# Kernel tuning notes

Measured on AMD Instinct MI355X. Metric: run time of the kernel, lower is better.

The kernel has to match this reference:

```python
import jax, jax.numpy as jnp
import numpy as np

N_NODES = 20000
SEQ_T = 24
EMB = 64
H_LSTM = 128
H_GCN = 128
OUT = 16
N_CAT = 20000
N_EDGE = 640000


def setup_inputs() -> dict:
    key = jax.random.key(0)
    ks = jax.random.split(key, 16)
    s = 0.05
    emb = jax.random.normal(ks[4], (N_CAT + 1, EMB), jnp.float32) * s
    emb = emb.at[0].set(0.0)  # padding_idx=0
    inp = {
        "x_tokens": jax.random.randint(ks[0], (N_NODES, SEQ_T), 0, N_CAT + 1, dtype=jnp.int32),
        "lengths": jax.random.randint(ks[1], (N_NODES,), 1, SEQ_T + 1, dtype=jnp.int32),
        "edge_index": jax.random.randint(ks[2], (2, N_EDGE), 0, N_NODES, dtype=jnp.int32),
        "edge_weight": jax.random.uniform(ks[3], (N_EDGE,), jnp.float32, 0.1, 1.0),
        "emb": emb,
        "W_ih": jax.random.normal(ks[5], (4 * H_LSTM, EMB), jnp.float32) * s,
        "W_hh": jax.random.normal(ks[6], (4 * H_LSTM, H_LSTM), jnp.float32) * s,
        "b_ih": jax.random.normal(ks[7], (4 * H_LSTM,), jnp.float32) * s,
        "b_hh": jax.random.normal(ks[8], (4 * H_LSTM,), jnp.float32) * s,
        "conv1_W": jax.random.normal(ks[9], (H_LSTM, H_GCN), jnp.float32) * s,
        "conv1_b": jax.random.normal(ks[10], (H_GCN,), jnp.float32) * s,
        "conv2_W": jax.random.normal(ks[11], (H_GCN, H_GCN), jnp.float32) * s,
        "conv2_b": jax.random.normal(ks[12], (H_GCN,), jnp.float32) * s,
        "fc_W": jax.random.normal(ks[13], (H_GCN, OUT), jnp.float32) * s,
        "fc_b": jax.random.normal(ks[14], (OUT,), jnp.float32) * s,
    }
    return inp


def _lstm_last(xseq, lengths, W_ih, W_hh, b):
    # xseq: [N, T, E]; unidirectional LSTM -> output at t=len-1 equals
    # pack_padded_sequence result (causality). PyTorch gate order: i, f, g, o.
    n = xseq.shape[0]
    h0 = jnp.zeros((n, H_LSTM), xseq.dtype)

    def step(carry, xt):
        h, c = carry
        z = xt @ W_ih.T + h @ W_hh.T + b  # [N, 4H]
        i, f, g, o = jnp.split(z, 4, axis=-1)
        c = jax.nn.sigmoid(f) * c + jax.nn.sigmoid(i) * jnp.tanh(g)
        h = jax.nn.sigmoid(o) * jnp.tanh(c)
        return (h, c), h

    _, hs = jax.lax.scan(step, (h0, h0), jnp.swapaxes(xseq, 0, 1))  # hs: [T, N, H]
    return hs[lengths - 1, jnp.arange(n)]  # [N, H]


def _gcn_conv(x, W, b, src, dst, w, n):
    # PyG GCNConv: self loops (weight 1) + symmetric normalization.
    h = x @ W  # [N, G]
    deg = jax.ops.segment_sum(w, dst, num_segments=n) + 1.0
    dinv = jax.lax.rsqrt(deg)
    norm = dinv[src] * w * dinv[dst]  # [E]
    agg = jax.ops.segment_sum(h[src] * norm[:, None], dst, num_segments=n)
    agg = agg + h * (dinv * dinv)[:, None]  # self-loop term
    return agg + b


def reference(x_tokens, lengths, edge_index, edge_weight, emb, W_ih, W_hh,
              b_ih, b_hh, conv1_W, conv1_b, conv2_W, conv2_b, fc_W, fc_b):
    n = x_tokens.shape[0]
    src, dst = edge_index[0], edge_index[1]
    xe = emb[x_tokens]  # [N, T, E]
    x = _lstm_last(xe, lengths, W_ih, W_hh, b_ih + b_hh)  # [N, H_LSTM]
    x = jax.nn.relu(_gcn_conv(x, conv1_W, conv1_b, src, dst, edge_weight, n))
    # dropout: identity (eval mode)
    x = jax.nn.relu(_gcn_conv(x, conv2_W, conv2_b, src, dst, edge_weight, n))
    return x @ fc_W + fc_b  # [N, OUT]
```

## Files before the change

### kernel.cpp

```cpp
#include <hip/hip_runtime.h>
#include <math.h>

#define N_NODES 20000
#define SEQ_T   24
#define EMBD    64
#define HL      128
#define OUTF    16
#define NEDGE   640000
#define G4      512
#define KTOT    192
#define ROWS    80
#define RF      5
#define NBLSTM  250
#define LDA     232
#define WSTRIDE 12288

#define NBCSR   250
#define EPB     (NEDGE/NBCSR)
#define NPB     (N_NODES/NBCSR)
#define CSRT    1024

#define CROWS   64
#define CRF     4
#define NCBLK   313
#define CPAD    136

typedef __bf16 bf16x8 __attribute__((ext_vector_type(8)));
typedef __bf16 bf16x2 __attribute__((ext_vector_type(2)));
typedef float  f32x4  __attribute__((ext_vector_type(4)));
typedef unsigned short u16;

__device__ __forceinline__ float4 ld4(const float* p){ return *reinterpret_cast<const float4*>(p); }
__device__ __forceinline__ void st4(float* p, float4 v){ *reinterpret_cast<float4*>(p) = v; }

#define LOG2E 1.44269504f

#define S_EMB   320016
#define S_WTP   (S_EMB + KTOT*G4)
#define S_C1    (S_WTP + 16384)
#define S_C2    (S_C1 + 16384)
#define S_BIAS  (S_C2 + G4)
#define PREPBLK ((S_BIAS + 255)/256)

__global__ __launch_bounds__(256) void prep_all(
    const float* __restrict__ emb,  __bf16* __restrict__ embb,
    const float* __restrict__ Wih,  const float* __restrict__ Whh,
    __bf16* __restrict__ WTp,
    const float* __restrict__ c1W,  __bf16* __restrict__ wc1b,
    const float* __restrict__ c2W,  __bf16* __restrict__ wc2b,
    const float* __restrict__ bi,   const float* __restrict__ bh,
    float* __restrict__ bs)
{
    int gid = blockIdx.x*256 + threadIdx.x;
    if (gid < S_EMB) {
        int i4 = gid*4;
        float4 v = ld4(emb + i4);
        embb[i4+0] = (__bf16)v.x;
        embb[i4+1] = (__bf16)v.y;
        embb[i4+2] = (__bf16)v.z;
        embb[i4+3] = (__bf16)v.w;
    } else if (gid < S_WTP) {
        int idx = gid - S_EMB;
        int ko = idx & 31;
        int c  = (idx >> 5) & 15;
        int gt = (idx >> 9) & 3;
        int kc = (idx >> 11) % 6;
        int w  = idx / WSTRIDE;
        int g  = gt*HL + w*16 + c;
        int kk = kc*32 + ko;
        float v = (kk < EMBD) ? Wih[g*EMBD + kk] : Whh[g*HL + (kk - EMBD)];
        WTp[idx] = (__bf16)v;
    } else if (gid < S_C2) {
        bool c2 = (gid >= S_C1);
        int idx = gid - (c2 ? S_C1 : S_WTP);
        const float* W = c2 ? c2W : c1W;
        __bf16* dst = c2 ? wc2b : wc1b;
        int ko = idx & 31;
        int c  = (idx >> 5) & 15;
        int kc = (idx >> 9) & 3;
        int w  = idx >> 11;
        int g  = w*16 + c;
        int k  = kc*32 + ko;
        dst[idx] = (__bf16)W[k*HL + g];
    } else if (gid < S_BIAS) {
        int i = gid - S_C2;
        bs[i] = bi[i] + bh[i];
    }
}

__global__ __launch_bounds__(CSRT) void csr_count(
    const int* __restrict__ esrc, const int* __restrict__ edst,
    const float* __restrict__ ew,
    int* __restrict__ rank, u16* __restrict__ gcnt, float* __restrict__ gdeg)
{
    __shared__ int   hist[N_NODES];
    __shared__ float fdeg[N_NODES];
    const int tid = threadIdx.x, bid = blockIdx.x;
    const int e0 = bid * EPB;

    uint4* h4 = reinterpret_cast<uint4*>(hist);
    uint4* f4 = reinterpret_cast<uint4*>(fdeg);
    for (int i = tid; i < N_NODES/4; i += CSRT) {
        h4[i] = make_uint4(0,0,0,0);
        f4[i] = make_uint4(0,0,0,0);
    }
    __syncthreads();

    #pragma unroll
    for (int k = 0; k < 3; ++k) {
        int i = tid + CSRT*k;
        if (k < 2 || i < EPB) {
            int e = e0 + i;
            int d = edst[e];
            rank[e] = atomicAdd(&hist[d], 1);
            atomicAdd(&fdeg[d], ew[e]);
        }
    }
    __syncthreads();

    for (int i = tid; i < N_NODES; i += CSRT) {
        gcnt[(size_t)bid*N_NODES + i] = (u16)hist[i];
        gdeg[(size_t)bid*N_NODES + i] = fdeg[i];
    }
}

__global__ __launch_bounds__(CSRT) void csr_scan(
    u16* __restrict__ gcnt, const float* __restrict__ gdeg,
    float* __restrict__ dinv, int* __restrict__ tot)
{
    __shared__ u16   ctile[NBCSR*NPB];
    __shared__ float dtile[NBCSR*NPB];
    const int tid = threadIdx.x, bid = blockIdx.x;
    const int nodes0 = bid * NPB;

    for (int idx = tid; idx < NBCSR*NPB; idx += CSRT) {
        int b = idx / NPB, i = idx - b*NPB;
        ctile[idx] = gcnt[(size_t)b*N_NODES + nodes0 + i];
        dtile[idx] = gdeg[(size_t)b*N_NODES + nodes0 + i];
    }
    __syncthreads();
    if (tid < NPB) {
        int run = 0; float dsum = 0.f;
        for (int b = 0; b < NBCSR; ++b) {
            int v = ctile[b*NPB + tid];
            ctile[b*NPB + tid] = (u16)run;
            run += v;
            dsum += dtile[b*NPB + tid];
        }
        tot[nodes0 + tid]  = run;
        dinv[nodes0 + tid] = rsqrtf(dsum + 1.0f);
    }
    __syncthreads();
    for (int idx = tid; idx < NBCSR*NPB; idx += CSRT) {
        int b = idx / NPB, i = idx - b*NPB;
        gcnt[(size_t)b*N_NODES + nodes0 + i] = ctile[idx];
    }
}

__global__ __launch_bounds__(256) void csr_rowstart(const int* __restrict__ tot,
                                                    int* __restrict__ row_start)
{
    __shared__ int part[NBCSR];
    const int t = threadIdx.x;
    if (t < NBCSR) {
        int s = 0;
        for (int i = 0; i < NPB; ++i) s += tot[t*NPB + i];
        part[t] = s;
    }
    __syncthreads();
    if (t == 0) {
        int run = 0;
        for (int b = 0; b < NBCSR; ++b) { int v = part[b]; part[b] = run; run += v; }
    }
    __syncthreads();
    if (t < NBCSR) {
        int base = part[t];
        for (int i = 0; i < NPB; ++i) {
            row_start[t*NPB + i] = base;
            base += tot[t*NPB + i];
        }
        if (t == NBCSR - 1) row_start[N_NODES] = base;
    }
}

__global__ __launch_bounds__(CSRT) void csr_fill(
    const int* __restrict__ esrc, const int* __restrict__ edst,
    const float* __restrict__ ew,
    const int* __restrict__ rank, const u16* __restrict__ gcnt,
    const int* __restrict__ row_start, const float* __restrict__ dinv,
    int* __restrict__ src_s, float* __restrict__ norm_s)
{
    const int tid = threadIdx.x, bid = blockIdx.x;
    const int e0 = bid * EPB;
    #pragma unroll
    for (int k = 0; k < 3; ++k) {
        int i = tid + CSRT*k;
        if (k < 2 || i < EPB) {
            int e = e0 + i;
            int d = edst[e], s = esrc[e];
            int pos = row_start[d] + (int)gcnt[(size_t)bid*N_NODES + d] + rank[e];
            src_s[pos]  = s;
            norm_s[pos] = dinv[s] * ew[e] * dinv[d];
        }
    }
}

__global__ __launch_bounds__(512, 2) void lstm_fused(
    const int* __restrict__ tokens, const int* __restrict__ lengths,
    const __bf16* __restrict__ embb, const __bf16* __restrict__ WTp,
    const float* __restrict__ bsum, const __bf16* __restrict__ wc1b,
    __bf16* __restrict__ ybf)
{
    __shared__ __align__(16) __bf16 a_lds[ROWS][LDA];
    __shared__ __align__(16) __bf16 hl_lds[ROWS][CPAD];
    __shared__ int tok_lds[ROWS*SEQ_T];
    __shared__ int len_lds[ROWS];

    const int tid = threadIdx.x;
    const int n0  = blockIdx.x * ROWS;
    const int w   = tid >> 6;
    const int l   = tid & 63;
    const int l15 = l & 15, l4 = l >> 4;

    #pragma unroll
    for (int i = 0; i < 4; ++i) {
        int idx = tid + 512*i;
        if (idx < ROWS*SEQ_T) tok_lds[idx] = tokens[n0*SEQ_T + idx];
    }
    if (tid < ROWS) len_lds[tid] = lengths[n0 + tid];

    #pragma unroll
    for (int i = 0; i < 3; ++i) {
        int idx = tid + 512*i;
        if (idx < ROWS*16) {
            int row = idx >> 4, s = idx & 15;
            *reinterpret_cast<uint4*>(&a_lds[row][EMBD + s*8]) = make_uint4(0,0,0,0);
        }
    }

    float bias_v[4];
    #pragma unroll
    for (int gt = 0; gt < 4; ++gt)
        bias_v[gt] = bsum[gt*HL + w*16 + l15];

    bf16x8 wreg[6][4];
    {
        const __bf16* wbase = WTp + (size_t)w * WSTRIDE;
        #pragma unroll
        for (int kc = 0; kc < 6; ++kc)
            #pragma unroll
            for (int gt = 0; gt < 4; ++gt)
                wreg[kc][gt] = *reinterpret_cast<const bf16x8*>(
                    &wbase[(size_t)(((kc*4 + gt)*16 + l15)*32) + l4*8]);
    }

    f32x4 acc[RF][4];
    float c_reg[RF][4];
    {
        f32x4 zz = {0.f,0.f,0.f,0.f};
        #pragma unroll
        for (int rf = 0; rf < RF; ++rf) {
            #pragma unroll
            for (int gt = 0; gt < 4; ++gt) acc[rf][gt] = zz;
            #pragma unroll
            for (int r = 0; r < 4; ++r) c_reg[rf][r] = 0.f;
        }
    }

    for (int t = 0; t < SEQ_T; ++t) {
        #pragma unroll
        for (int i = 0; i < 2; ++i) {
            int idx = tid + 512*i;
            if (idx < ROWS*8) {
                int row = idx >> 3, sl = idx & 7;
                int tok = tok_lds[row*SEQ_T + t];
                *reinterpret_cast<uint4*>(&a_lds[row][sl*8]) =
                    *reinterpret_cast<const uint4*>(&embb[(size_t)tok*EMBD + sl*8]);
            }
        }
        __syncthreads();

        #pragma unroll
        for (int kc = 0; kc < 6; ++kc)
            #pragma unroll
            for (int rf = 0; rf < RF; ++rf) {
                bf16x8 af = *reinterpret_cast<const bf16x8*>(
                    &a_lds[rf*16 + l15][kc*32 + l4*8]);
                #pragma unroll
                for (int gt = 0; gt < 4; ++gt)
                    acc[rf][gt] = __builtin_amdgcn_mfma_f32_16x16x32_bf16(
                        af, wreg[kc][gt], acc[rf][gt], 0, 0, 0);
            }
        __syncthreads();

        #pragma unroll
        for (int rf = 0; rf < RF; ++rf) {
            f32x4 zi4 = acc[rf][0], zf4 = acc[rf][1];
            f32x4 zg4 = acc[rf][2], zo4 = acc[rf][3];
            #pragma unroll
            for (int r = 0; r < 4; ++r) {
                int row = rf*16 + l4*4 + r;
                float zi = zi4[r] + bias_v[0];
                float zf = zf4[r] + bias_v[1];
                float zg = zg4[r] + bias_v[2];
                float zo = zo4[r] + bias_v[3];
                float ef = __builtin_amdgcn_exp2f(-LOG2E*zf);
                float ei = __builtin_amdgcn_exp2f(-LOG2E*zi);
                float eg = __builtin_amdgcn_exp2f(2.0f*LOG2E*zg);
                float sf  = __builtin_amdgcn_rcpf(1.0f + ef);
                float rig = __builtin_amdgcn_rcpf((1.0f + ei)*(eg + 1.0f));
                float cc = sf*c_reg[rf][r] + (eg - 1.0f)*rig;
                c_reg[rf][r] = cc;
                float eo = __builtin_amdgcn_exp2f(-LOG2E*zo);
                float ec = __builtin_amdgcn_exp2f(2.0f*LOG2E*cc);
                float rh = __builtin_amdgcn_rcpf((1.0f + eo)*(ec + 1.0f));
                float h = (ec - 1.0f)*rh;
                int j = w*16 + l15;
                a_lds[row][EMBD + j] = (__bf16)h;
                if (len_lds[row] == t + 1)
                    hl_lds[row][j] = (__bf16)h;
            }
            f32x4 zz = {0.f,0.f,0.f,0.f};
            acc[rf][0] = zz; acc[rf][1] = zz; acc[rf][2] = zz; acc[rf][3] = zz;
        }
    }

    __syncthreads();

    {
        bf16x8 wb1[4];
        #pragma unroll
        for (int kc = 0; kc < 4; ++kc)
            wb1[kc] = *reinterpret_cast<const bf16x8*>(
                &wc1b[(size_t)(((w*4 + kc)*16 + l15)*32) + l4*8]);
        int j = w*16 + l15;
        #pragma unroll
        for (int rf = 0; rf < RF; ++rf) {
            f32x4 a2 = {0.f,0.f,0.f,0.f};
            #pragma unroll
            for (int kc = 0; kc < 4; ++kc) {
                bf16x8 af = *reinterpret_cast<const bf16x8*>(
                    &hl_lds[rf*16 + l15][kc*32 + l4*8]);
                a2 = __builtin_amdgcn_mfma_f32_16x16x32_bf16(af, wb1[kc], a2, 0, 0, 0);
            }
            #pragma unroll
            for (int r = 0; r < 4; ++r)
                ybf[(size_t)(n0 + rf*16 + l4*4 + r)*HL + j] = (__bf16)a2[r];
        }
    }
}

__global__ __launch_bounds__(512) void gemm_mfma(const __bf16* __restrict__ xb,
                                                 const __bf16* __restrict__ Wb,
                                                 __bf16* __restrict__ y, int N)
{
    __shared__ __align__(16) __bf16 a_lds[CROWS][CPAD];
    const int tid = threadIdx.x;
    const int n0 = blockIdx.x * CROWS;
    const int w = tid >> 6, l = tid & 63;
    const int l15 = l & 15, l4 = l >> 4;

    {
        int row = tid >> 3, sl = tid & 7;
        int n = n0 + row;
        uint4 v0 = make_uint4(0,0,0,0), v1 = make_uint4(0,0,0,0);
        if (n < N) {
            v0 = *reinterpret_cast<const uint4*>(xb + (size_t)n*HL + sl*16);
            v1 = *reinterpret_cast<const uint4*>(xb + (size_t)n*HL + sl*16 + 8);
        }
        *reinterpret_cast<uint4*>(&a_lds[row][sl*16])     = v0;
        *reinterpret_cast<uint4*>(&a_lds[row][sl*16 + 8]) = v1;
    }

    bf16x8 wb[4];
    #pragma unroll
    for (int kc = 0; kc < 4; ++kc)
        wb[kc] = *reinterpret_cast<const bf16x8*>(
            &Wb[(size_t)(((w*4 + kc)*16 + l15)*32) + l4*8]);

    f32x4 acc[CRF];
    {
        f32x4 zz = {0.f,0.f,0.f,0.f};
        #pragma unroll
        for (int rf = 0; rf < CRF; ++rf) acc[rf] = zz;
    }
    __syncthreads();

    #pragma unroll
    for (int kc = 0; kc < 4; ++kc)
        #pragma unroll
        for (int rf = 0; rf < CRF; ++rf) {
            bf16x8 af = *reinterpret_cast<const bf16x8*>(
                &a_lds[rf*16 + l15][kc*32 + l4*8]);
            acc[rf] = __builtin_amdgcn_mfma_f32_16x16x32_bf16(af, wb[kc], acc[rf], 0, 0, 0);
        }

    int j = w*16 + l15;
    #pragma unroll
    for (int rf = 0; rf < CRF; ++rf)
        #pragma unroll
        for (int r = 0; r < 4; ++r) {
            int n = n0 + rf*16 + l4*4 + r;
            if (n < N) y[(size_t)n*HL + j] = (__bf16)acc[rf][r];
        }
}

template<int MODE>
__global__ __launch_bounds__(256) void gcn_gather_k(
    const int* __restrict__ row_start, const int* __restrict__ src_s,
    const float* __restrict__ norm_s, const float* __restrict__ dinv,
    const __bf16* __restrict__ y, const float* __restrict__ b,
    __bf16* __restrict__ outb,
    const float* __restrict__ fcW, const float* __restrict__ fcb,
    float* __restrict__ fcout, int N)
{
    __shared__ float xrow[4][HL];
    const int tid = threadIdx.x;
    int gt = blockIdx.x*256 + tid;
    int n = gt >> 6, lane = gt & 63;
    bool act = (n < N);
    float ax = 0.f, ay = 0.f;
    if (act) {
        const int beg = row_start[n], end = row_start[n+1];
        int p = beg;
        for (; p + 4 <= end; p += 4) {
            int   s0 = src_s[p+0], s1 = src_s[p+1], s2 = src_s[p+2], s3 = src_s[p+3];
            float w0 = norm_s[p+0], w1 = norm_s[p+1], w2 = norm_s[p+2], w3 = norm_s[p+3];
            bf16x2 v0 = *reinterpret_cast<const bf16x2*>(y + (size_t)s0*HL + lane*2);
            bf16x2 v1 = *reinterpret_cast<const bf16x2*>(y + (size_t)s1*HL + lane*2);
            bf16x2 v2 = *reinterpret_cast<const bf16x2*>(y + (size_t)s2*HL + lane*2);
            bf16x2 v3 = *reinterpret_cast<const bf16x2*>(y + (size_t)s3*HL + lane*2);
            ax = fmaf(w0, (float)v0[0], ax); ay = fmaf(w0, (float)v0[1], ay);
            ax = fmaf(w1, (float)v1[0], ax); ay = fmaf(w1, (float)v1[1], ay);
            ax = fmaf(w2, (float)v2[0], ax); ay = fmaf(w2, (float)v2[1], ay);
            ax = fmaf(w3, (float)v3[0], ax); ay = fmaf(w3, (float)v3[1], ay);
        }
        for (; p < end; ++p) {
            int s = src_s[p];
            float nrm = norm_s[p];
            bf16x2 v = *reinterpret_cast<const bf16x2*>(y + (size_t)s*HL + lane*2);
            ax = fmaf(nrm, (float)v[0], ax);
            ay = fmaf(nrm, (float)v[1], ay);
        }
        float di = dinv[n];
        float sl = di*di;
        bf16x2 vs = *reinterpret_cast<const bf16x2*>(y + (size_t)n*HL + lane*2);
        ax = fmaf(sl, (float)vs[0], ax);
        ay = fmaf(sl, (float)vs[1], ay);
        float2 bb = *reinterpret_cast<const float2*>(b + lane*2);
        ax = fmaxf(ax + bb.x, 0.f);
        ay = fmaxf(ay + bb.y, 0.f);
    }
    if (MODE == 1) {
        if (act) {
            bf16x2 o;
            o[0] = (__bf16)ax; o[1] = (__bf16)ay;
            *reinterpret_cast<bf16x2*>(outb + (size_t)n*HL + lane*2) = o;
        }
    } else {
        int nq = tid >> 6;
        xrow[nq][lane*2]     = ax;
        xrow[nq][lane*2 + 1] = ay;
        __syncthreads();
        if (tid < 64) {
            int q = tid >> 4, o = tid & 15;
            int nn = blockIdx.x*4 + q;
            if (nn < N) {
                float a = fcb[o];
                #pragma unroll 8
                for (int k = 0; k < HL; ++k)
                    a = fmaf(xrow[q][k], fcW[k*OUTF + o], a);
                fcout[(size_t)nn*OUTF + o] = a;
            }
        }
    }
}

extern "C" void kernel_launch(void* const* d_in, const int* in_sizes, int n_in,
                              void* d_out, int out_size, void* d_ws, size_t ws_size,
                              hipStream_t stream)
{
    const int*   x_tokens = (const int*)d_in[0];
    const int*   lengths  = (const int*)d_in[1];
    const int*   eidx     = (const int*)d_in[2];
    const float* ew       = (const float*)d_in[3];
    const float* emb      = (const float*)d_in[4];
    const float* W_ih     = (const float*)d_in[5];
    const float* W_hh     = (const float*)d_in[6];
    const float* b_ih     = (const float*)d_in[7];
    const float* b_hh     = (const float*)d_in[8];
    const float* c1W      = (const float*)d_in[9];
    const float* c1b      = (const float*)d_in[10];
    const float* c2W      = (const float*)d_in[11];
    const float* c2b      = (const float*)d_in[12];
    const float* fcW      = (const float*)d_in[13];
    const float* fcb      = (const float*)d_in[14];
    float* out = (float*)d_out;

    const int* esrc = eidx;
    const int* edst = eidx + NEDGE;

    char* ws = (char*)d_ws;
    size_t off = 0;
    auto take = [&](size_t bytes) -> char* {
        char* p = ws + off;
        off = (off + bytes + 255) & ~(size_t)255;
        return p;
    };
    __bf16* embb = (__bf16*)take((size_t)(N_NODES + 1) * EMBD * sizeof(__bf16));
    __bf16* WTp  = (__bf16*)take((size_t)KTOT * G4 * sizeof(__bf16));
    __bf16* wc1b = (__bf16*)take((size_t)HL * HL * sizeof(__bf16));
    __bf16* wc2b = (__bf16*)take((size_t)HL * HL * sizeof(__bf16));
    float* bsum  = (float*)take((size_t)G4 * sizeof(float));
    __bf16* ybf  = (__bf16*)take((size_t)N_NODES * HL * sizeof(__bf16));
    __bf16* x2b  = (__bf16*)take((size_t)N_NODES * HL * sizeof(__bf16));
    float* dinvb = (float*)take((size_t)N_NODES * sizeof(float));
    int*   rankb = (int*)  take((size_t)NEDGE * sizeof(int));
    u16*   gcnt  = (u16*)  take((size_t)NBCSR * N_NODES * sizeof(u16));
    float* gdeg  = (float*)take((size_t)NBCSR * N_NODES * sizeof(float));
    int*   totb  = (int*)  take((size_t)N_NODES * sizeof(int));
    int*   rowst = (int*)  take((size_t)(N_NODES + 1) * sizeof(int));
    int*   srcS  = (int*)  take((size_t)NEDGE * sizeof(int));
    float* nrmS  = (float*)take((size_t)NEDGE * sizeof(float));

    prep_all<<<PREPBLK, 256, 0, stream>>>(emb, embb, W_ih, W_hh, WTp,
                                          c1W, wc1b, c2W, wc2b, b_ih, b_hh, bsum);

    csr_count<<<NBCSR, CSRT, 0, stream>>>(esrc, edst, ew, rankb, gcnt, gdeg);
    csr_scan<<<NBCSR, CSRT, 0, stream>>>(gcnt, gdeg, dinvb, totb);
    csr_rowstart<<<1, 256, 0, stream>>>(totb, rowst);
    csr_fill<<<NBCSR, CSRT, 0, stream>>>(esrc, edst, ew, rankb, gcnt, rowst,
                                         dinvb, srcS, nrmS);

    lstm_fused<<<NBLSTM, 512, 0, stream>>>(x_tokens, lengths, embb, WTp, bsum,
                                           wc1b, ybf);

    const int gathBlocks = (N_NODES*64 + 255)/256;

    gcn_gather_k<1><<<gathBlocks, 256, 0, stream>>>(rowst, srcS, nrmS, dinvb, ybf,
                                                    c1b, x2b, nullptr, nullptr, nullptr, N_NODES);
    gemm_mfma<<<NCBLK, 512, 0, stream>>>(x2b, wc2b, ybf, N_NODES);
    gcn_gather_k<2><<<gathBlocks, 256, 0, stream>>>(rowst, srcS, nrmS, dinvb, ybf,
                                                    c2b, nullptr, fcW, fcb, out, N_NODES);
}
```

Before: 286.8 us.

## Fuse first GCN gather into second-layer GEMM and shrink CSR build blocks

The layer-1 gather with bias and ReLU is merged with the conv2 MFMA GEMM in one kernel, so each block gathers 64 rows into LDS and multiplies them there instead of writing and rereading an intermediate bf16 buffer and paying an extra launch. The CSR count and fill kernels now use 64 edge blocks instead of 250, which shrinks the per-block count/degree arrays the scan reads, and per-edge ranks are stored as 16-bit. The cost is lower parallelism: the fused gather runs on only 313 blocks with one wave per row in sequence, and the count kernel has fewer, longer blocks.

```diff
diff --git a/kernel.cpp b/kernel.cpp
--- a/kernel.cpp
+++ b/kernel.cpp
@@ -15,9 +15,10 @@
 #define LDA     232
 #define WSTRIDE 12288
 
-#define NBCSR   250
-#define EPB     (NEDGE/NBCSR)
-#define NPB     (N_NODES/NBCSR)
+#define NB1     64
+#define EPB1    (NEDGE/NB1)
+#define NBSC    250
+#define NPB     (N_NODES/NBSC)
 #define CSRT    1024
 
 #define CROWS   64
@@ -31,7 +32,6 @@
 typedef unsigned short u16;
 
 __device__ __forceinline__ float4 ld4(const float* p){ return *reinterpret_cast<const float4*>(p); }
-__device__ __forceinline__ void st4(float* p, float4 v){ *reinterpret_cast<float4*>(p) = v; }
 
 #define LOG2E 1.44269504f
 
@@ -91,12 +91,12 @@
 __global__ __launch_bounds__(CSRT) void csr_count(
     const int* __restrict__ esrc, const int* __restrict__ edst,
     const float* __restrict__ ew,
-    int* __restrict__ rank, u16* __restrict__ gcnt, float* __restrict__ gdeg)
+    u16* __restrict__ rank, u16* __restrict__ gcnt, float* __restrict__ gdeg)
 {
     __shared__ int   hist[N_NODES];
     __shared__ float fdeg[N_NODES];
     const int tid = threadIdx.x, bid = blockIdx.x;
-    const int e0 = bid * EPB;
+    const int e0 = bid * EPB1;
 
     uint4* h4 = reinterpret_cast<uint4*>(hist);
     uint4* f4 = reinterpret_cast<uint4*>(fdeg);
@@ -106,15 +106,11 @@
     }
     __syncthreads();
 
-    #pragma unroll
-    for (int k = 0; k < 3; ++k) {
-        int i = tid + CSRT*k;
-        if (k < 2 || i < EPB) {
-            int e = e0 + i;
-            int d = edst[e];
-            rank[e] = atomicAdd(&hist[d], 1);
-            atomicAdd(&fdeg[d], ew[e]);
-        }
+    for (int i = tid; i < EPB1; i += CSRT) {
+        int e = e0 + i;
+        int d = edst[e];
+        rank[e] = (u16)atomicAdd(&hist[d], 1);
+        atomicAdd(&fdeg[d], ew[e]);
     }
     __syncthreads();
 
@@ -128,12 +124,12 @@
     u16* __restrict__ gcnt, const float* __restrict__ gdeg,
     float* __restrict__ dinv, int* __restrict__ tot)
 {
-    __shared__ u16   ctile[NBCSR*NPB];
-    __shared__ float dtile[NBCSR*NPB];
+    __shared__ u16   ctile[NB1*NPB];
+    __shared__ float dtile[NB1*NPB];
     const int tid = threadIdx.x, bid = blockIdx.x;
     const int nodes0 = bid * NPB;
 
-    for (int idx = tid; idx < NBCSR*NPB; idx += CSRT) {
+    for (int idx = tid; idx < NB1*NPB; idx += CSRT) {
         int b = idx / NPB, i = idx - b*NPB;
         ctile[idx] = gcnt[(size_t)b*N_NODES + nodes0 + i];
         dtile[idx] = gdeg[(size_t)b*N_NODES + nodes0 + i];
@@ -141,7 +137,8 @@
     __syncthreads();
     if (tid < NPB) {
         int run = 0; float dsum = 0.f;
-        for (int b = 0; b < NBCSR; ++b) {
+        #pragma unroll 4
+        for (int b = 0; b < NB1; ++b) {
             int v = ctile[b*NPB + tid];
             ctile[b*NPB + tid] = (u16)run;
             run += v;
@@ -151,7 +148,7 @@
         dinv[nodes0 + tid] = rsqrtf(dsum + 1.0f);
     }
     __syncthreads();
-    for (int idx = tid; idx < NBCSR*NPB; idx += CSRT) {
+    for (int idx = tid; idx < NB1*NPB; idx += CSRT) {
         int b = idx / NPB, i = idx - b*NPB;
         gcnt[(size_t)b*N_NODES + nodes0 + i] = ctile[idx];
     }
@@ -160,9 +157,9 @@
 __global__ __launch_bounds__(256) void csr_rowstart(const int* __restrict__ tot,
                                                     int* __restrict__ row_start)
 {
-    __shared__ int part[NBCSR];
+    __shared__ int part[NBSC];
     const int t = threadIdx.x;
-    if (t < NBCSR) {
+    if (t < NBSC) {
         int s = 0;
         for (int i = 0; i < NPB; ++i) s += tot[t*NPB + i];
         part[t] = s;
@@ -170,38 +167,34 @@
     __syncthreads();
     if (t == 0) {
         int run = 0;
-        for (int b = 0; b < NBCSR; ++b) { int v = part[b]; part[b] = run; run += v; }
-    }
-    __syncthreads();
-    if (t < NBCSR) {
+        for (int b = 0; b < NBSC; ++b) { int v = part[b]; part[b] = run; run += v; }
+    }
+    __syncthreads();
+    if (t < NBSC) {
         int base = part[t];
         for (int i = 0; i < NPB; ++i) {
             row_start[t*NPB + i] = base;
             base += tot[t*NPB + i];
         }
-        if (t == NBCSR - 1) row_start[N_NODES] = base;
+        if (t == NBSC - 1) row_start[N_NODES] = base;
     }
 }
 
 __global__ __launch_bounds__(CSRT) void csr_fill(
     const int* __restrict__ esrc, const int* __restrict__ edst,
     const float* __restrict__ ew,
-    const int* __restrict__ rank, const u16* __restrict__ gcnt,
+    const u16* __restrict__ rank, const u16* __restrict__ gcnt,
     const int* __restrict__ row_start, const float* __restrict__ dinv,
     int* __restrict__ src_s, float* __restrict__ norm_s)
 {
     const int tid = threadIdx.x, bid = blockIdx.x;
-    const int e0 = bid * EPB;
-    #pragma unroll
-    for (int k = 0; k < 3; ++k) {
-        int i = tid + CSRT*k;
-        if (k < 2 || i < EPB) {
-            int e = e0 + i;
-            int d = edst[e], s = esrc[e];
-            int pos = row_start[d] + (int)gcnt[(size_t)bid*N_NODES + d] + rank[e];
-            src_s[pos]  = s;
-            norm_s[pos] = dinv[s] * ew[e] * dinv[d];
-        }
+    const int e0 = bid * EPB1;
+    for (int i = tid; i < EPB1; i += CSRT) {
+        int e = e0 + i;
+        int d = edst[e], s = esrc[e];
+        int pos = row_start[d] + (int)gcnt[(size_t)bid*N_NODES + d] + (int)rank[e];
+        src_s[pos]  = s;
+        norm_s[pos] = dinv[s] * ew[e] * dinv[d];
     }
 }
 
@@ -350,67 +343,100 @@
     }
 }
 
-__global__ __launch_bounds__(512) void gemm_mfma(const __bf16* __restrict__ xb,
-                                                 const __bf16* __restrict__ Wb,
-                                                 __bf16* __restrict__ y, int N)
+__global__ __launch_bounds__(256) void gcn_gather_gemm(
+    const int* __restrict__ row_start, const int* __restrict__ src_s,
+    const float* __restrict__ norm_s, const float* __restrict__ dinv,
+    const __bf16* __restrict__ y, const float* __restrict__ b,
+    const __bf16* __restrict__ wc2b, __bf16* __restrict__ y2, int N)
 {
     __shared__ __align__(16) __bf16 a_lds[CROWS][CPAD];
     const int tid = threadIdx.x;
     const int n0 = blockIdx.x * CROWS;
-    const int w = tid >> 6, l = tid & 63;
-    const int l15 = l & 15, l4 = l >> 4;
-
-    {
-        int row = tid >> 3, sl = tid & 7;
+    const int wv = tid >> 6, ln = tid & 63;
+    const int l15 = ln & 15, l4 = ln >> 4;
+
+    for (int r = 0; r < 16; ++r) {
+        int row = wv + 4*r;
         int n = n0 + row;
-        uint4 v0 = make_uint4(0,0,0,0), v1 = make_uint4(0,0,0,0);
+        float ax = 0.f, ay = 0.f;
         if (n < N) {
-            v0 = *reinterpret_cast<const uint4*>(xb + (size_t)n*HL + sl*16);
-            v1 = *reinterpret_cast<const uint4*>(xb + (size_t)n*HL + sl*16 + 8);
-        }
-        *reinterpret_cast<uint4*>(&a_lds[row][sl*16])     = v0;
-        *reinterpret_cast<uint4*>(&a_lds[row][sl*16 + 8]) = v1;
-    }
-
-    bf16x8 wb[4];
+            const int beg = row_start[n], end = row_start[n+1];
+            int p = beg;
+            for (; p + 4 <= end; p += 4) {
+                int   s0 = src_s[p+0], s1 = src_s[p+1], s2 = src_s[p+2], s3 = src_s[p+3];
+                float w0 = norm_s[p+0], w1 = norm_s[p+1], w2 = norm_s[p+2], w3 = norm_s[p+3];
+                bf16x2 v0 = *reinterpret_cast<const bf16x2*>(y + (size_t)s0*HL + ln*2);
+                bf16x2 v1 = *reinterpret_cast<const bf16x2*>(y + (size_t)s1*HL + ln*2);
+                bf16x2 v2 = *reinterpret_cast<const bf16x2*>(y + (size_t)s2*HL + ln*2);
+                bf16x2 v3 = *reinterpret_cast<const bf16x2*>(y + (size_t)s3*HL + ln*2);
+                ax = fmaf(w0, (float)v0[0], ax); ay = fmaf(w0, (float)v0[1], ay);
+                ax = fmaf(w1, (float)v1[0], ax); ay = fmaf(w1, (float)v1[1], ay);
+                ax = fmaf(w2, (float)v2[0], ax); ay = fmaf(w2, (float)v2[1], ay);
+                ax = fmaf(w3, (float)v3[0], ax); ay = fmaf(w3, (float)v3[1], ay);
+            }
+            for (; p < end; ++p) {
+                int s = src_s[p];
+                float nrm = norm_s[p];
+                bf16x2 v = *reinterpret_cast<const bf16x2*>(y + (size_t)s*HL + ln*2);
+                ax = fmaf(nrm, (float)v[0], ax);
+                ay = fmaf(nrm, (float)v[1], ay);
+            }
+            float di = dinv[n];
+            float sl = di*di;
+            bf16x2 vs = *reinterpret_cast<const bf16x2*>(y + (size_t)n*HL + ln*2);
+            ax = fmaf(sl, (float)vs[0], ax);
+            ay = fmaf(sl, (float)vs[1], ay);
+            float2 bb = *reinterpret_cast<const float2*>(b + ln*2);
+            ax = fmaxf(ax + bb.x, 0.f);
+            ay = fmaxf(ay + bb.y, 0.f);
+        }
+        bf16x2 o;
+        o[0] = (__bf16)ax; o[1] = (__bf16)ay;
+        *reinterpret_cast<bf16x2*>(&a_lds[row][ln*2]) = o;
+    }
+    __syncthreads();
+
+    bf16x8 wb[4][2];
     #pragma unroll
-    for (int kc = 0; kc < 4; ++kc)
-        wb[kc] = *reinterpret_cast<const bf16x8*>(
-            &Wb[(size_t)(((w*4 + kc)*16 + l15)*32) + l4*8]);
-
-    f32x4 acc[CRF];
+    for (int q = 0; q < 2; ++q) {
+        int cg = wv*2 + q;
+        #pragma unroll
+        for (int kc = 0; kc < 4; ++kc)
+            wb[kc][q] = *reinterpret_cast<const bf16x8*>(
+                &wc2b[(size_t)(((cg*4 + kc)*16 + l15)*32) + l4*8]);
+    }
+    f32x4 acc[CRF][2];
     {
         f32x4 zz = {0.f,0.f,0.f,0.f};
         #pragma unroll
-        for (int rf = 0; rf < CRF; ++rf) acc[rf] = zz;
-    }
-    __syncthreads();
-
+        for (int rf = 0; rf < CRF; ++rf) { acc[rf][0] = zz; acc[rf][1] = zz; }
+    }
     #pragma unroll
     for (int kc = 0; kc < 4; ++kc)
         #pragma unroll
         for (int rf = 0; rf < CRF; ++rf) {
             bf16x8 af = *reinterpret_cast<const bf16x8*>(
                 &a_lds[rf*16 + l15][kc*32 + l4*8]);
-            acc[rf] = __builtin_amdgcn_mfma_f32_16x16x32_bf16(af, wb[kc], acc[rf], 0, 0, 0);
-        }
-
-    int j = w*16 + l15;
+            acc[rf][0] = __builtin_amdgcn_mfma_f32_16x16x32_bf16(af, wb[kc][0], acc[rf][0], 0, 0, 0);
+            acc[rf][1] = __builtin_amdgcn_mfma_f32_16x16x32_bf16(af, wb[kc][1], acc[rf][1], 0, 0, 0);
+        }
     #pragma unroll
     for (int rf = 0; rf < CRF; ++rf)
         #pragma unroll
-        for (int r = 0; r < 4; ++r) {
-            int n = n0 + rf*16 + l4*4 + r;
-            if (n < N) y[(size_t)n*HL + j] = (__bf16)acc[rf][r];
-        }
-}
-
-template<int MODE>
-__global__ __launch_bounds__(256) void gcn_gather_k(
+        for (int q = 0; q < 2; ++q) {
+            int j = (wv*2 + q)*16 + l15;
+            #pragma unroll
+            for (int r = 0; r < 4; ++r) {
+                int n = n0 + rf*16 + l4*4 + r;
+                if (n < N) y2[(size_t)n*HL + j] = (__bf16)acc[rf][q][r];
+            }
+        }
+}
+
+__global__ __launch_bounds__(256) void gcn_gather_fc(
     const int* __restrict__ row_start, const int* __restrict__ src_s,
     const float* __restrict__ norm_s, const float* __restrict__ dinv,
     const __bf16* __restrict__ y, const float* __restrict__ b,
-    __bf16* __restrict__ outb,
     const float* __restrict__ fcW, const float* __restrict__ fcb,
     float* __restrict__ fcout, int N)
 {
@@ -451,27 +477,19 @@
         ax = fmaxf(ax + bb.x, 0.f);
         ay = fmaxf(ay + bb.y, 0.f);
     }
-    if (MODE == 1) {
-        if (act) {
-            bf16x2 o;
-            o[0] = (__bf16)ax; o[1] = (__bf16)ay;
-            *reinterpret_cast<bf16x2*>(outb + (size_t)n*HL + lane*2) = o;
-        }
-    } else {
-        int nq = tid >> 6;
-        xrow[nq][lane*2]     = ax;
-        xrow[nq][lane*2 + 1] = ay;
-        __syncthreads();
-        if (tid < 64) {
-            int q = tid >> 4, o = tid & 15;
-            int nn = blockIdx.x*4 + q;
-            if (nn < N) {
-                float a = fcb[o];
-                #pragma unroll 8
-                for (int k = 0; k < HL; ++k)
-                    a = fmaf(xrow[q][k], fcW[k*OUTF + o], a);
-                fcout[(size_t)nn*OUTF + o] = a;
-            }
+    int nq = tid >> 6;
+    xrow[nq][lane*2]     = ax;
+    xrow[nq][lane*2 + 1] = ay;
+    __syncthreads();
+    if (tid < 64) {
+        int q = tid >> 4, o = tid & 15;
+        int nn = blockIdx.x*4 + q;
+        if (nn < N) {
+            float a = fcb[o];
+            #pragma unroll 8
+            for (int k = 0; k < HL; ++k)
+                a = fmaf(xrow[q][k], fcW[k*OUTF + o], a);
+            fcout[(size_t)nn*OUTF + o] = a;
         }
     }
 }
@@ -515,9 +533,9 @@
     __bf16* ybf  = (__bf16*)take((size_t)N_NODES * HL * sizeof(__bf16));
     __bf16* x2b  = (__bf16*)take((size_t)N_NODES * HL * sizeof(__bf16));
     float* dinvb = (float*)take((size_t)N_NODES * sizeof(float));
-    int*   rankb = (int*)  take((size_t)NEDGE * sizeof(int));
-    u16*   gcnt  = (u16*)  take((size_t)NBCSR * N_NODES * sizeof(u16));
-    float* gdeg  = (float*)take((size_t)NBCSR * N_NODES * sizeof(float));
+    u16*   rankb = (u16*)  take((size_t)NEDGE * sizeof(u16));
+    u16*   gcnt  = (u16*)  take((size_t)NB1 * N_NODES * sizeof(u16));
+    float* gdeg  = (float*)take((size_t)NB1 * N_NODES * sizeof(float));
     int*   totb  = (int*)  take((size_t)N_NODES * sizeof(int));
     int*   rowst = (int*)  take((size_t)(N_NODES + 1) * sizeof(int));
     int*   srcS  = (int*)  take((size_t)NEDGE * sizeof(int));
@@ -526,20 +544,19 @@
     prep_all<<<PREPBLK, 256, 0, stream>>>(emb, embb, W_ih, W_hh, WTp,
                                           c1W, wc1b, c2W, wc2b, b_ih, b_hh, bsum);
 
-    csr_count<<<NBCSR, CSRT, 0, stream>>>(esrc, edst, ew, rankb, gcnt, gdeg);
-    csr_scan<<<NBCSR, CSRT, 0, stream>>>(gcnt, gdeg, dinvb, totb);
+    csr_count<<<NB1, CSRT, 0, stream>>>(esrc, edst, ew, rankb, gcnt, gdeg);
+    csr_scan<<<NBSC, CSRT, 0, stream>>>(gcnt, gdeg, dinvb, totb);
     csr_rowstart<<<1, 256, 0, stream>>>(totb, rowst);
-    csr_fill<<<NBCSR, CSRT, 0, stream>>>(esrc, edst, ew, rankb, gcnt, rowst,
-                                         dinvb, srcS, nrmS);
+    csr_fill<<<NB1, CSRT, 0, stream>>>(esrc, edst, ew, rankb, gcnt, rowst,
+                                       dinvb, srcS, nrmS);
 
     lstm_fused<<<NBLSTM, 512, 0, stream>>>(x_tokens, lengths, embb, WTp, bsum,
                                            wc1b, ybf);
 
+    gcn_gather_gemm<<<NCBLK, 256, 0, stream>>>(rowst, srcS, nrmS, dinvb, ybf,
+                                               c1b, wc2b, x2b, N_NODES);
+
     const int gathBlocks = (N_NODES*64 + 255)/256;
-
-    gcn_gather_k<1><<<gathBlocks, 256, 0, stream>>>(rowst, srcS, nrmS, dinvb, ybf,
-                                                    c1b, x2b, nullptr, nullptr, nullptr, N_NODES);
-    gemm_mfma<<<NCBLK, 512, 0, stream>>>(x2b, wc2b, ybf, N_NODES);
-    gcn_gather_k<2><<<gathBlocks, 256, 0, stream>>>(rowst, srcS, nrmS, dinvb, ybf,
-                                                    c2b, nullptr, fcW, fcb, out, N_NODES);
-}
+    gcn_gather_fc<<<gathBlocks, 256, 0, stream>>>(rowst, srcS, nrmS, dinvb, x2b,
+                                                  c2b, fcW, fcb, out, N_NODES);
+}
```

Measured after the change: 376.9 us. +31.4%, slower.
